# Kernel optimization log

Measured on AMD Instinct MI355X. Metric: run time of the kernel, lower is better.

## Reference

```python
import jax, jax.numpy as jnp
import numpy as np

TAU = 0.6      # similarity threshold in tokenwise_interpolation
TOPK = 3       # top-k candidates
ALPHA = 0.5    # interpolation weight (module default self.alpha)
EPS = 1e-12    # F.normalize eps


def _l2norm(x):
    n = jnp.linalg.norm(x, axis=-1, keepdims=True)
    return x / jnp.maximum(n, EPS)


def _mh_rms(x, gamma):
    # SparseMultiHeadRMSNorm: F.normalize over last dim, * gamma * sqrt(dim)
    dim = x.shape[-1]
    return _l2norm(x) * gamma * (dim ** 0.5)


def _match_and_copy(sim, k_flat, v_flat, k_side, v_side):
    topv, topi = jax.lax.top_k(sim, min(TOPK, sim.shape[1]))
    valid = topv[:, 0] > TAU                      # [N]
    kg = k_side[topi[:, 0]]                       # gather best match
    vg = v_side[topi[:, 0]]
    k_out = jnp.where(valid[:, None], kg, k_flat)
    v_out = jnp.where(valid[:, None], vg, v_flat)
    return k_out, v_out


def setup_inputs() -> dict:
    key = jax.random.key(0)
    ks = jax.random.split(key, 8)
    N, H, C = 4096, 16, 64
    D = H * C
    inp = {
        'x':  jax.random.normal(ks[0], (N, D), jnp.float32),
        'k0': jax.random.normal(ks[1], (N, H, C), jnp.float32),
        'v0': jax.random.normal(ks[2], (N, H, C), jnp.float32),
        'k1': jax.random.normal(ks[3], (N, H, C), jnp.float32),
        'v1': jax.random.normal(ks[4], (N, H, C), jnp.float32),
        'W_qkv': jax.random.normal(ks[5], (D, 3 * D), jnp.float32) * 0.02,
        'b_qkv': jnp.zeros((3 * D,), jnp.float32),
        'gamma_q': jnp.ones((H, C), jnp.float32),
        'gamma_k': jnp.ones((H, C), jnp.float32),
        'W_out': jax.random.normal(ks[6], (D, D), jnp.float32) * 0.02,
        'b_out': jnp.zeros((D,), jnp.float32),
    }
    return inp


def reference(x, k0, v0, k1, v1, W_qkv, b_qkv, gamma_q, gamma_k, W_out, b_out):
    N, D = x.shape
    H, C = gamma_q.shape

    # fused QKV projection -> (N, 3, H, C)
    qkv = (x @ W_qkv + b_qkv).reshape(N, 3, H, C)
    q, k, v = qkv[:, 0], qkv[:, 1], qkv[:, 2]

    # q RMS norm
    q = _mh_rms(q, gamma_q)

    # tokenwise interpolation: cosine top-k matching against stores
    k_flat, v_flat = k.reshape(N, D), v.reshape(N, D)
    k0f, v0f = k0.reshape(-1, D), v0.reshape(-1, D)
    k1f, v1f = k1.reshape(-1, D), v1.reshape(-1, D)
    kbn = _l2norm(k_flat)
    sim0 = kbn @ _l2norm(k0f).T        # [N, N0]
    sim1 = kbn @ _l2norm(k1f).T        # [N, N1]
    k_out0, v_out0 = _match_and_copy(sim0, k_flat, v_flat, k0f, v0f)
    k_out1, v_out1 = _match_and_copy(sim1, k_flat, v_flat, k1f, v1f)

    # combine with residual and detached norm rescale
    combined_k = (1.0 - ALPHA) * k_out0 + ALPHA * k_out1 + k_flat
    sk = jax.lax.stop_gradient(jnp.linalg.norm(k_flat) / jnp.linalg.norm(combined_k))
    k_out = (combined_k * sk).reshape(N, H, C)
    combined_v = (1.0 - ALPHA) * v_out0 + ALPHA * v_out1 + v_flat
    sv = jax.lax.stop_gradient(jnp.linalg.norm(v_flat) / jnp.linalg.norm(combined_v))
    v_out = (combined_v * sv).reshape(N, H, C)

    # k RMS norm after interpolation
    k_out = _mh_rms(k_out, gamma_k)

    # full scaled dot-product attention (single sparse batch => one sequence)
    scores = jnp.einsum('nhc,mhc->hnm', q, k_out) / (C ** 0.5)
    attn = jax.nn.softmax(scores, axis=-1)
    h = jnp.einsum('hnm,mhc->nhc', attn, v_out).reshape(N, D)

    return h @ W_out + b_out
```

## Files before the change

kernel.cpp:

```cpp
#include <hip/hip_runtime.h>
#include <math.h>

#define TAU_F 0.6f

typedef short short8 __attribute__((ext_vector_type(8)));
typedef float floatx4 __attribute__((ext_vector_type(4)));
typedef int   intx4  __attribute__((ext_vector_type(4)));

__device__ __forceinline__ ushort f2bf(float f) {
    unsigned u = __float_as_uint(f);
    u += 0x7FFF + ((u >> 16) & 1);
    return (ushort)(u >> 16);
}
__device__ __forceinline__ float bf2f(ushort h) {
    return __uint_as_float(((unsigned)h) << 16);
}
__device__ __forceinline__ int swz(int row, int j, int mask) { return j ^ (row & mask); }

__device__ __forceinline__ unsigned cvt_pk_bf16(float lo, float hi) {
    unsigned r;
    asm("v_cvt_pk_bf16_f32 %0, %1, %2" : "=v"(r) : "v"(lo), "v"(hi));
    return r;
}
__device__ __forceinline__ float exp2_fast(float x) {
    float r; asm("v_exp_f32 %0, %1" : "=v"(r) : "v"(x)); return r;
}

template<int CPR, int SC, int NW = 4>
__device__ __forceinline__ void stage_swz(void* lds, const char* g, int rowstride_bytes,
                                          int w, int lane)
{
    #pragma unroll
    for (int p = 0; p < (SC + NW - 1) / NW; ++p) {
        int sc = w + p * NW;
        if (SC % NW != 0 && sc >= SC) break;
        int LC = sc * 64 + lane;
        int r = LC / CPR;
        int s = LC % CPR;
        int j = s ^ (r & (CPR - 1));
        const char* gp = g + (size_t)r * rowstride_bytes + j * 16;
        __builtin_amdgcn_global_load_lds(
            (const __attribute__((address_space(1))) void*)gp,
            (__attribute__((address_space(3))) void*)((char*)lds + sc * 1024), 16, 0, 0);
    }
}

__global__ __launch_bounds__(256) void gemm_nt_kernel(
    const ushort* __restrict__ Ah, int lda,
    const ushort* __restrict__ Bh, int ldb,
    const float* __restrict__ bias, float* __restrict__ C, int ldc, int K)
{
    __shared__ __align__(16) ushort As_h[128 * 32];
    __shared__ __align__(16) ushort Bs_h[128 * 32];
    const int tid = threadIdx.x;
    const int w = tid >> 6, lane = tid & 63;
    const int quad = lane >> 4, c15 = lane & 15;
    const int wm = w >> 1, wn = w & 1;
    const int bm = blockIdx.y * 128, bn = blockIdx.x * 128;

    floatx4 acc[4][4];
    #pragma unroll
    for (int i = 0; i < 4; i++)
        #pragma unroll
        for (int j = 0; j < 4; j++) acc[i][j] = (floatx4){0.f, 0.f, 0.f, 0.f};

    const char* Ab = (const char*)(Ah + (size_t)bm * lda);
    const char* Bb = (const char*)(Bh + (size_t)bn * ldb);

    for (int k0 = 0; k0 < K; k0 += 32) {
        stage_swz<4, 8>(As_h, Ab + k0 * 2, lda * 2, w, lane);
        stage_swz<4, 8>(Bs_h, Bb + k0 * 2, ldb * 2, w, lane);
        __syncthreads();
        short8 a_h[4], b_h[4];
        #pragma unroll
        for (int mt = 0; mt < 4; mt++) {
            int row = wm * 64 + mt * 16 + c15;
            a_h[mt] = *(const short8*)&As_h[row * 32 + swz(row, quad, 3) * 8];
        }
        #pragma unroll
        for (int nt = 0; nt < 4; nt++) {
            int row = wn * 64 + nt * 16 + c15;
            b_h[nt] = *(const short8*)&Bs_h[row * 32 + swz(row, quad, 3) * 8];
        }
        #pragma unroll
        for (int mt = 0; mt < 4; mt++)
            #pragma unroll
            for (int nt = 0; nt < 4; nt++)
                acc[mt][nt] = __builtin_amdgcn_mfma_f32_16x16x32_bf16(a_h[mt], b_h[nt], acc[mt][nt], 0, 0, 0);
        __syncthreads();
    }
    #pragma unroll
    for (int mt = 0; mt < 4; mt++)
        #pragma unroll
        for (int nt = 0; nt < 4; nt++) {
            int col = bn + wn * 64 + nt * 16 + c15;
            float bs = bias ? bias[col] : 0.f;
            #pragma unroll
            for (int r = 0; r < 4; r++) {
                int row = bm + wm * 64 + mt * 16 + quad * 4 + r;
                C[(size_t)row * ldc + col] = acc[mt][nt][r] + bs;
            }
        }
}

__global__ __launch_bounds__(256) void gemm_nt64_kernel(
    const ushort* __restrict__ Ah, int lda,
    const ushort* __restrict__ Bh, int ldb,
    const float* __restrict__ bias, float* __restrict__ C, int ldc, int K)
{
    __shared__ __align__(16) ushort As_h[128 * 32];
    __shared__ __align__(16) ushort Bs_h[64 * 32];
    const int tid = threadIdx.x;
    const int w = tid >> 6, lane = tid & 63;
    const int quad = lane >> 4, c15 = lane & 15;
    const int wm = w >> 1, wn = w & 1;
    const int bm = blockIdx.y * 128, bn = blockIdx.x * 64;

    floatx4 acc[4][2];
    #pragma unroll
    for (int i = 0; i < 4; i++)
        #pragma unroll
        for (int j = 0; j < 2; j++) acc[i][j] = (floatx4){0.f, 0.f, 0.f, 0.f};

    const char* Ab = (const char*)(Ah + (size_t)bm * lda);
    const char* Bb = (const char*)(Bh + (size_t)bn * ldb);

    for (int k0 = 0; k0 < K; k0 += 32) {
        stage_swz<4, 8>(As_h, Ab + k0 * 2, lda * 2, w, lane);
        stage_swz<4, 4>(Bs_h, Bb + k0 * 2, ldb * 2, w, lane);
        __syncthreads();
        short8 a_h[4], b_h[2];
        #pragma unroll
        for (int mt = 0; mt < 4; mt++) {
            int row = wm * 64 + mt * 16 + c15;
            a_h[mt] = *(const short8*)&As_h[row * 32 + swz(row, quad, 3) * 8];
        }
        #pragma unroll
        for (int nt = 0; nt < 2; nt++) {
            int row = wn * 32 + nt * 16 + c15;
            b_h[nt] = *(const short8*)&Bs_h[row * 32 + swz(row, quad, 3) * 8];
        }
        #pragma unroll
        for (int mt = 0; mt < 4; mt++)
            #pragma unroll
            for (int nt = 0; nt < 2; nt++)
                acc[mt][nt] = __builtin_amdgcn_mfma_f32_16x16x32_bf16(a_h[mt], b_h[nt], acc[mt][nt], 0, 0, 0);
        __syncthreads();
    }
    #pragma unroll
    for (int mt = 0; mt < 4; mt++)
        #pragma unroll
        for (int nt = 0; nt < 2; nt++) {
            int col = bn + wn * 32 + nt * 16 + c15;
            float bs = bias ? bias[col] : 0.f;
            #pragma unroll
            for (int r = 0; r < 4; r++) {
                int row = bm + wm * 64 + mt * 16 + quad * 4 + r;
                C[(size_t)row * ldc + col] = acc[mt][nt][r] + bs;
            }
        }
}

__global__ __launch_bounds__(256) void simmax_i8(
    const char* __restrict__ A, const char* __restrict__ B,
    float* __restrict__ pval, int* __restrict__ pidx)
{
    __shared__ __align__(16) char As_b[128 * 64];
    __shared__ __align__(16) char Bs_b[128 * 64];
    __shared__ float redv[128][2];
    __shared__ int   redi[128][2];
    const int tid = threadIdx.x;
    const int w = tid >> 6, lane = tid & 63;
    const int quad = lane >> 4, c15 = lane & 15;
    const int wm = w >> 1, wn = w & 1;
    const int bm = blockIdx.y * 128, bn = blockIdx.x * 128;

    intx4 acc[4][4];
    #pragma unroll
    for (int i = 0; i < 4; i++)
        #pragma unroll
        for (int j = 0; j < 4; j++) acc[i][j] = (intx4){0, 0, 0, 0};

    const char* Ab = A + (size_t)bm * 1024;
    const char* Bb = B + (size_t)bn * 1024;

    for (int k0 = 0; k0 < 1024; k0 += 64) {
        stage_swz<4, 8>(As_b, Ab + k0, 1024, w, lane);
        stage_swz<4, 8>(Bs_b, Bb + k0, 1024, w, lane);
        __syncthreads();
        intx4 a_f[4], b_f[4];
        #pragma unroll
        for (int mt = 0; mt < 4; mt++) {
            int row = wm * 64 + mt * 16 + c15;
            a_f[mt] = *(const intx4*)&As_b[row * 64 + swz(row, quad, 3) * 16];
        }
        #pragma unroll
        for (int nt = 0; nt < 4; nt++) {
            int row = wn * 64 + nt * 16 + c15;
            b_f[nt] = *(const intx4*)&Bs_b[row * 64 + swz(row, quad, 3) * 16];
        }
        #pragma unroll
        for (int mt = 0; mt < 4; mt++)
            #pragma unroll
            for (int nt = 0; nt < 4; nt++)
                acc[mt][nt] = __builtin_amdgcn_mfma_i32_16x16x64_i8(a_f[mt], b_f[nt], acc[mt][nt], 0, 0, 0);
        __syncthreads();
    }
    const float isc = 1.0f / 16129.0f;
    #pragma unroll
    for (int mt = 0; mt < 4; mt++)
        #pragma unroll
        for (int r = 0; r < 4; r++) {
            float bv = -1e30f; int bi = 0;
            #pragma unroll
            for (int nt = 0; nt < 4; nt++) {
                float v = (float)acc[mt][nt][r] * isc;
                int col = bn + wn * 64 + nt * 16 + c15;
                if (v > bv) { bv = v; bi = col; }
            }
            #pragma unroll
            for (int m = 1; m < 16; m <<= 1) {
                float ov = __shfl_xor(bv, m, 64);
                int   oi = __shfl_xor(bi, m, 64);
                if (ov > bv || (ov == bv && oi < bi)) { bv = ov; bi = oi; }
            }
            if (c15 == 0) {
                int row = wm * 64 + mt * 16 + quad * 4 + r;
                redv[row][wn] = bv; redi[row][wn] = bi;
            }
        }
    __syncthreads();
    if (tid < 128) {
        float v0 = redv[tid][0], v1 = redv[tid][1];
        int   i0 = redi[tid][0], i1 = redi[tid][1];
        bool t = (v1 > v0) || (v1 == v0 && i1 < i0);
        pval[(size_t)blockIdx.x * 4096 + bm + tid] = t ? v1 : v0;
        pidx[(size_t)blockIdx.x * 4096 + bm + tid] = t ? i1 : i0;
    }
}

__global__ void simreduce2_kernel(const float* __restrict__ pval, const int* __restrict__ pidx,
                                  float* __restrict__ bv0, int* __restrict__ bi0,
                                  float* __restrict__ bv1, int* __restrict__ bi1)
{
    const int n = blockIdx.x * 256 + threadIdx.x;
    float best = -1e30f; int besti = 0x7fffffff;
    for (int c = 0; c < 32; c++) {
        float v = pval[(size_t)c * 4096 + n]; int ix = pidx[(size_t)c * 4096 + n];
        if (v > best || (v == best && ix < besti)) { best = v; besti = ix; }
    }
    bv0[n] = best; bi0[n] = besti;
    best = -1e30f; besti = 0x7fffffff;
    for (int c = 32; c < 64; c++) {
        float v = pval[(size_t)c * 4096 + n]; int ix = pidx[(size_t)c * 4096 + n];
        if (v > best || (v == best && ix < besti)) { best = v; besti = ix; }
    }
    bv1[n] = best; bi1[n] = besti - 4096;
}

__global__ __launch_bounds__(256) void xconv_kernel(const float* __restrict__ s,
                                                    ushort* __restrict__ dh)
{
    const int i = blockIdx.x * 256 + threadIdx.x;
    float4 v = ((const float4*)s)[i];
    ushort4 h;
    h.x = f2bf(v.x); h.y = f2bf(v.y); h.z = f2bf(v.z); h.w = f2bf(v.w);
    ((ushort4*)dh)[i] = h;
}

__global__ __launch_bounds__(256) void wtrans_kernel(const float* __restrict__ src, int R, int Cc,
                                                     ushort* __restrict__ dh)
{
    __shared__ float t[64][65];
    const int tid = threadIdx.x;
    const int c0 = blockIdx.x * 64, r0 = blockIdx.y * 64;
    #pragma unroll
    for (int i = 0; i < 16; i++) {
        int lin = i * 256 + tid;
        int rr = lin >> 6, cc = lin & 63;
        t[rr][cc] = src[(size_t)(r0 + rr) * Cc + c0 + cc];
    }
    __syncthreads();
    #pragma unroll
    for (int i = 0; i < 16; i++) {
        int lin = i * 256 + tid;
        int cc2 = lin >> 6, rr2 = lin & 63;
        dh[(size_t)(c0 + cc2) * R + r0 + rr2] = f2bf(t[rr2][cc2]);
    }
}

__device__ __forceinline__ char q127(float v) {
    float c = fminf(fmaxf(v * 127.0f, -127.0f), 127.0f);
    return (char)__float2int_rn(c);
}

__global__ __launch_bounds__(256) void prep_kernel(const float* __restrict__ QKV,
                                                   const float* __restrict__ k0,
                                                   const float* __restrict__ k1,
                                                   const float* __restrict__ gamma_q,
                                                   char* __restrict__ kq,
                                                   char* __restrict__ k01q,
                                                   ushort* __restrict__ Qbh)
{
    const int n = blockIdx.x, t = threadIdx.x, y = blockIdx.y;
    if (y == 3) {
        float4 v = ((const float4*)(QKV + (size_t)n * 3072))[t];
        float hs = v.x * v.x + v.y * v.y + v.z * v.z + v.w * v.w;
        #pragma unroll
        for (int m = 1; m < 16; m <<= 1) hs += __shfl_xor(hs, m, 64);
        float inv = 8.0f / fmaxf(sqrtf(hs), 1e-12f);
        float4 g = ((const float4*)gamma_q)[t];
        const int h = t >> 4;
        size_t o = ((size_t)h * 4096 + n) * 64 + 4 * (t & 15);
        ushort4 hh;
        hh.x = f2bf(v.x * inv * g.x);
        hh.y = f2bf(v.y * inv * g.y);
        hh.z = f2bf(v.z * inv * g.z);
        hh.w = f2bf(v.w * inv * g.w);
        *(ushort4*)(Qbh + o) = hh;
        return;
    }
    const float* src; int ld; char* dst;
    if (y == 0)      { src = QKV + 1024; ld = 3072; dst = kq; }
    else if (y == 1) { src = k0; ld = 1024; dst = k01q; }
    else             { src = k1; ld = 1024; dst = k01q + (size_t)4096 * 1024; }
    float4 v = *(const float4*)(src + (size_t)n * ld + 4 * t);
    float ss = v.x * v.x + v.y * v.y + v.z * v.z + v.w * v.w;
    #pragma unroll
    for (int off = 32; off; off >>= 1) ss += __shfl_xor(ss, off, 64);
    __shared__ float wsum[4];
    if ((t & 63) == 0) wsum[t >> 6] = ss;
    __syncthreads();
    float inv = 1.0f / fmaxf(sqrtf(wsum[0] + wsum[1] + wsum[2] + wsum[3]), 1e-12f);
    char4 o;
    o.x = q127(v.x * inv); o.y = q127(v.y * inv);
    o.z = q127(v.z * inv); o.w = q127(v.w * inv);
    *(char4*)(dst + (size_t)n * 1024 + 4 * t) = o;
}

__global__ __launch_bounds__(256) void combine_kernel(
    const float* __restrict__ QKV,
    const float* __restrict__ k0, const float* __restrict__ v0,
    const float* __restrict__ k1, const float* __restrict__ v1,
    const float* __restrict__ bv0, const int* __restrict__ bi0,
    const float* __restrict__ bv1, const int* __restrict__ bi1,
    const float* __restrict__ gamma_k,
    ushort* __restrict__ CKh,
    float* __restrict__ CV, float* __restrict__ pps)
{
    const int n = blockIdx.x, t = threadIdx.x;
    const bool va0 = bv0[n] > TAU_F; const int i0 = bi0[n];
    const bool va1 = bv1[n] > TAU_F; const int i1 = bi1[n];
    float4 kf = ((const float4*)(QKV + (size_t)n * 3072 + 1024))[t];
    float4 vf = ((const float4*)(QKV + (size_t)n * 3072 + 2048))[t];
    float4 kg0 = va0 ? ((const float4*)(k0 + (size_t)i0 * 1024))[t] : kf;
    float4 vg0 = va0 ? ((const float4*)(v0 + (size_t)i0 * 1024))[t] : vf;
    float4 kg1 = va1 ? ((const float4*)(k1 + (size_t)i1 * 1024))[t] : kf;
    float4 vg1 = va1 ? ((const float4*)(v1 + (size_t)i1 * 1024))[t] : vf;
    float4 ck, cv;
    ck.x = 0.5f * kg0.x + 0.5f * kg1.x + kf.x;
    ck.y = 0.5f * kg0.y + 0.5f * kg1.y + kf.y;
    ck.z = 0.5f * kg0.z + 0.5f * kg1.z + kf.z;
    ck.w = 0.5f * kg0.w + 0.5f * kg1.w + kf.w;
    cv.x = 0.5f * vg0.x + 0.5f * vg1.x + vf.x;
    cv.y = 0.5f * vg0.y + 0.5f * vg1.y + vf.y;
    cv.z = 0.5f * vg0.z + 0.5f * vg1.z + vf.z;
    cv.w = 0.5f * vg0.w + 0.5f * vg1.w + vf.w;
    ((float4*)(CV + (size_t)n * 1024))[t] = cv;
    float s0 = vf.x * vf.x + vf.y * vf.y + vf.z * vf.z + vf.w * vf.w;
    float s1 = cv.x * cv.x + cv.y * cv.y + cv.z * cv.z + cv.w * cv.w;
    #pragma unroll
    for (int off = 32; off; off >>= 1) {
        s0 += __shfl_xor(s0, off, 64);
        s1 += __shfl_xor(s1, off, 64);
    }
    __shared__ float w0[4], w1[4];
    if ((t & 63) == 0) { w0[t >> 6] = s0; w1[t >> 6] = s1; }
    float hs = ck.x * ck.x + ck.y * ck.y + ck.z * ck.z + ck.w * ck.w;
    #pragma unroll
    for (int m = 1; m < 16; m <<= 1) hs += __shfl_xor(hs, m, 64);
    float inv = 8.0f / fmaxf(sqrtf(hs), 1e-12f);
    float4 g = ((const float4*)gamma_k)[t];
    const int h = t >> 4;
    size_t o = ((size_t)h * 4096 + n) * 64 + 4 * (t & 15);
    ushort4 hh;
    hh.x = f2bf(ck.x * inv * g.x);
    hh.y = f2bf(ck.y * inv * g.y);
    hh.z = f2bf(ck.z * inv * g.z);
    hh.w = f2bf(ck.w * inv * g.w);
    *(ushort4*)(CKh + o) = hh;
    __syncthreads();
    if (t == 0) {
        pps[n]        = w0[0] + w0[1] + w0[2] + w0[3];
        pps[4096 + n] = w1[0] + w1[1] + w1[2] + w1[3];
    }
}

__global__ __launch_bounds__(256) void sumred_kernel(const float* __restrict__ pps,
                                                     float* __restrict__ ss)
{
    const int t = threadIdx.x;
    float a = 0.f, b = 0.f;
    #pragma unroll 4
    for (int i = t; i < 4096; i += 256) { a += pps[i]; b += pps[4096 + i]; }
    #pragma unroll
    for (int off = 32; off; off >>= 1) {
        a += __shfl_xor(a, off, 64);
        b += __shfl_xor(b, off, 64);
    }
    __shared__ float sa[4], sb[4];
    if ((t & 63) == 0) { sa[t >> 6] = a; sb[t >> 6] = b; }
    __syncthreads();
    if (t == 0) {
        ss[0] = sa[0] + sa[1] + sa[2] + sa[3];
        ss[1] = sb[0] + sb[1] + sb[2] + sb[3];
    }
}

__global__ __launch_bounds__(256) void vt_kernel(const float* __restrict__ CV,
                                                 const float* __restrict__ ss,
                                                 ushort* __restrict__ Vt)
{
    __shared__ float t[64][65];
    const float sv = sqrtf(ss[0] / ss[1]);
    const int tid = threadIdx.x;
    const int n0 = blockIdx.x * 64, d0 = blockIdx.y * 64;
    #pragma unroll
    for (int i = 0; i < 16; i++) {
        int lin = i * 256 + tid;
        int r = lin >> 6, c = lin & 63;
        t[r][c] = CV[(size_t)(n0 + r) * 1024 + d0 + c];
    }
    __syncthreads();
    #pragma unroll
    for (int i = 0; i < 16; i++) {
        int lin = i * 256 + tid;
        int dr = lin >> 6, nc = lin & 63;
        Vt[(size_t)(d0 + dr) * 4096 + n0 + nc] = f2bf(t[nc][dr] * sv);
    }
}

__global__ __launch_bounds__(512, 6) void attn_mfma(
    const ushort* __restrict__ Qh,
    const ushort* __restrict__ Kh,
    const ushort* __restrict__ Vt,
    ushort* __restrict__ Hb)
{
    __shared__ __align__(16) ushort Ks[2][64 * 64];
    __shared__ __align__(16) ushort Vs[2][64 * 64];
    __shared__ __align__(16) ushort Ps[128 * 64];
    const int h = blockIdx.y;
    const int n0 = blockIdx.x * 128;
    const int tid = threadIdx.x;
    const int w = tid >> 6, lane = tid & 63;
    const int quad = lane >> 4, c15 = lane & 15;

    short8 qf[2];
    #pragma unroll
    for (int kh = 0; kh < 2; kh++)
        qf[kh] = *(const short8*)(Qh + ((size_t)h * 4096 + n0 + w * 16 + c15) * 64 + kh * 32 + quad * 8);

    floatx4 po[4];
    #pragma unroll
    for (int nt = 0; nt < 4; nt++) po[nt] = (floatx4){0.f, 0.f, 0.f, 0.f};
    float lsum = 0.f;

    const float KSC = 0.18033688011112042f;
    const float KBI = -12.262907847556189f;

    const int prow = w * 16 + c15;
    const ushort* Kbase = Kh + (size_t)h * 4096 * 64;
    const ushort* Vbase = Vt + (size_t)h * 64 * 4096;

    stage_swz<8, 8, 8>(Ks[0], (const char*)(Kbase + 0), 128, w, lane);
    stage_swz<8, 8, 8>(Vs[0], (const char*)(Vbase + 0), 8192, w, lane);
    __syncthreads();

    int cur = 0;
    for (int it = 0; it < 64; ++it) {
        if (it + 1 < 64) {
            const int m1 = (it + 1) * 64;
            stage_swz<8, 8, 8>(Ks[cur ^ 1], (const char*)(Kbase + (size_t)m1 * 64), 128, w, lane);
            stage_swz<8, 8, 8>(Vs[cur ^ 1], (const char*)(Vbase + m1), 8192, w, lane);
        }
        const ushort* Kc = Ks[cur];
        const ushort* Vc = Vs[cur];

        floatx4 s[4];
        #pragma unroll
        for (int nt = 0; nt < 4; nt++) {
            int rk = nt * 16 + c15;
            short8 ka = *(const short8*)&Kc[rk * 64 + swz(rk, quad, 7) * 8];
            short8 kb = *(const short8*)&Kc[rk * 64 + swz(rk, 4 + quad, 7) * 8];
            floatx4 z = (floatx4){0.f, 0.f, 0.f, 0.f};
            z = __builtin_amdgcn_mfma_f32_16x16x32_bf16(ka, qf[0], z, 0, 0, 0);
            z = __builtin_amdgcn_mfma_f32_16x16x32_bf16(kb, qf[1], z, 0, 0, 0);
            s[nt] = z;
        }
        #pragma unroll
        for (int nt = 0; nt < 4; nt++) {
            float p0 = exp2_fast(fmaf(s[nt][0], KSC, KBI));
            float p1 = exp2_fast(fmaf(s[nt][1], KSC, KBI));
            float p2 = exp2_fast(fmaf(s[nt][2], KSC, KBI));
            float p3 = exp2_fast(fmaf(s[nt][3], KSC, KBI));
            lsum += (p0 + p1) + (p2 + p3);
            uint2 pk;
            pk.x = cvt_pk_bf16(p0, p1);
            pk.y = cvt_pk_bf16(p2, p3);
            int ch = (nt * 4 + quad) ^ ((prow & 7) << 1);
            *(uint2*)&Ps[prow * 64 + ch * 4] = pk;
        }
        __builtin_amdgcn_wave_barrier();
        #pragma unroll
        for (int kb2 = 0; kb2 < 2; kb2++) {
            short8 pa = *(const short8*)&Ps[prow * 64 + swz(prow, kb2 * 4 + quad, 7) * 8];
            #pragma unroll
            for (int nt = 0; nt < 4; nt++) {
                int dr = nt * 16 + c15;
                int j = kb2 * 4 + quad;
                short8 vb = *(const short8*)&Vc[dr * 64 + swz(dr, j, 7) * 8];
                po[nt] = __builtin_amdgcn_mfma_f32_16x16x32_bf16(pa, vb, po[nt], 0, 0, 0);
            }
        }
        __syncthreads();
        cur ^= 1;
    }
    float l = lsum;
    l += __shfl_xor(l, 16, 64);
    l += __shfl_xor(l, 32, 64);
    #pragma unroll
    for (int r = 0; r < 4; r++) {
        float lr = __shfl(l, quad * 4 + r, 64);
        float inv = 1.0f / lr;
        int row = n0 + w * 16 + quad * 4 + r;
        #pragma unroll
        for (int nt = 0; nt < 4; nt++)
            Hb[(size_t)row * 1024 + h * 64 + nt * 16 + c15] = f2bf(po[nt][r] * inv);
    }
}

extern "C" void kernel_launch(void* const* d_in, const int* in_sizes, int n_in,
                              void* d_out, int out_size, void* d_ws, size_t ws_size,
                              hipStream_t stream)
{
    const float* x       = (const float*)d_in[0];
    const float* k0      = (const float*)d_in[1];
    const float* v0      = (const float*)d_in[2];
    const float* k1      = (const float*)d_in[3];
    const float* v1      = (const float*)d_in[4];
    const float* W_qkv   = (const float*)d_in[5];
    const float* b_qkv   = (const float*)d_in[6];
    const float* gamma_q = (const float*)d_in[7];
    const float* gamma_k = (const float*)d_in[8];
    const float* W_out   = (const float*)d_in[9];
    const float* b_out   = (const float*)d_in[10];
    float* out = (float*)d_out;

    char* W = (char*)d_ws;
    float*  QKV = (float*)(W + 0);
    ushort* Vt  = (ushort*)(W + 0);
    ushort* Hb  = (ushort*)(W + 8388608);
    ushort* Qbh = (ushort*)(W + 50331648);
    ushort* xh   = (ushort*)(W + 67108864);
    ushort* Wqh  = (ushort*)(W + 67108864 + 8388608);
    char*   kq   = (char*)(W + 67108864);
    char*   k01q = (char*)(W + 67108864 + 4194304);
    float*  pval = (float*)(W + 67108864 + 25165824);
    int*    pidx = (int*)  (W + 67108864 + 26214400);
    float*  CV   = (float*)(W + 67108864);
    ushort* CKh  = (ushort*)(W + 67108864 + 16777216);
    ushort* Wob  = (ushort*)(W + 67108864);
    float* bv0  = (float*)(W + 100663296);
    int*   bi0  = (int*)  (W + 100663296 + 16384);
    float* bv1  = (float*)(W + 100663296 + 32768);
    int*   bi1  = (int*)  (W + 100663296 + 49152);
    float* ssum = (float*)(W + 100663296 + 65536);
    float* pps  = (float*)(W + 100663296 + 131072);

    xconv_kernel<<<4096, 256, 0, stream>>>(x, xh);
    wtrans_kernel<<<dim3(48, 16), 256, 0, stream>>>(W_qkv, 1024, 3072, Wqh);
    gemm_nt_kernel<<<dim3(24, 32), 256, 0, stream>>>(xh, 1024, Wqh, 1024,
                                                     b_qkv, QKV, 3072, 1024);
    prep_kernel<<<dim3(4096, 4), 256, 0, stream>>>(QKV, k0, k1, gamma_q, kq, k01q, Qbh);
    simmax_i8<<<dim3(64, 32), 256, 0, stream>>>(kq, k01q, pval, pidx);
    simreduce2_kernel<<<16, 256, 0, stream>>>(pval, pidx, bv0, bi0, bv1, bi1);
    combine_kernel<<<4096, 256, 0, stream>>>(QKV, k0, v0, k1, v1, bv0, bi0, bv1, bi1,
                                             gamma_k, CKh, CV, pps);
    sumred_kernel<<<1, 256, 0, stream>>>(pps, ssum);
    vt_kernel<<<dim3(64, 16), 256, 0, stream>>>(CV, ssum, Vt);
    wtrans_kernel<<<dim3(16, 16), 256, 0, stream>>>(W_out, 1024, 1024, Wob);
    attn_mfma<<<dim3(32, 16), 512, 0, stream>>>(Qbh, CKh, Vt, Hb);
    gemm_nt64_kernel<<<dim3(16, 32), 256, 0, stream>>>(Hb, 1024, Wob, 1024,
                                                       b_out, out, 1024, 1024);
}
```

Before: 404.3 us.

## Process two 16-row query groups per wave in attention, halving block threads

The attention kernel now runs 4 waves of 256 threads per block instead of 8 waves, and each wave handles 32 query rows as two 16-row groups. Each K and V fragment read from LDS therefore feeds two MFMAs. This roughly halves LDS read traffic per FLOP and the staging work per thread stays the same in total. In exchange it needs more registers per wave (double accumulators and scores), has fewer waves to hide latency, and the launch bounds change to (256,2), which may lower occupancy.

```diff
diff --git a/kernel.cpp b/kernel.cpp
--- a/kernel.cpp
+++ b/kernel.cpp
@@ -440,7 +440,7 @@
     }
 }
 
-__global__ __launch_bounds__(512, 6) void attn_mfma(
+__global__ __launch_bounds__(256, 2) void attn_mfma(
     const ushort* __restrict__ Qh,
     const ushort* __restrict__ Kh,
     const ushort* __restrict__ Vt,
@@ -455,87 +455,105 @@
     const int w = tid >> 6, lane = tid & 63;
     const int quad = lane >> 4, c15 = lane & 15;
 
-    short8 qf[2];
-    #pragma unroll
-    for (int kh = 0; kh < 2; kh++)
-        qf[kh] = *(const short8*)(Qh + ((size_t)h * 4096 + n0 + w * 16 + c15) * 64 + kh * 32 + quad * 8);
-
-    floatx4 po[4];
-    #pragma unroll
-    for (int nt = 0; nt < 4; nt++) po[nt] = (floatx4){0.f, 0.f, 0.f, 0.f};
-    float lsum = 0.f;
+    short8 qf[2][2];
+    #pragma unroll
+    for (int g = 0; g < 2; g++)
+        #pragma unroll
+        for (int kh = 0; kh < 2; kh++)
+            qf[g][kh] = *(const short8*)(Qh + ((size_t)h * 4096 + n0 + w * 32 + g * 16 + c15) * 64
+                                         + kh * 32 + quad * 8);
+
+    floatx4 po[2][4];
+    #pragma unroll
+    for (int g = 0; g < 2; g++)
+        #pragma unroll
+        for (int nt = 0; nt < 4; nt++) po[g][nt] = (floatx4){0.f, 0.f, 0.f, 0.f};
+    float lsum[2] = {0.f, 0.f};
 
     const float KSC = 0.18033688011112042f;
     const float KBI = -12.262907847556189f;
 
-    const int prow = w * 16 + c15;
+    const int pr0 = w * 32 + c15;
     const ushort* Kbase = Kh + (size_t)h * 4096 * 64;
     const ushort* Vbase = Vt + (size_t)h * 64 * 4096;
 
-    stage_swz<8, 8, 8>(Ks[0], (const char*)(Kbase + 0), 128, w, lane);
-    stage_swz<8, 8, 8>(Vs[0], (const char*)(Vbase + 0), 8192, w, lane);
+    stage_swz<8, 8, 4>(Ks[0], (const char*)(Kbase + 0), 128, w, lane);
+    stage_swz<8, 8, 4>(Vs[0], (const char*)(Vbase + 0), 8192, w, lane);
     __syncthreads();
 
     int cur = 0;
     for (int it = 0; it < 64; ++it) {
         if (it + 1 < 64) {
             const int m1 = (it + 1) * 64;
-            stage_swz<8, 8, 8>(Ks[cur ^ 1], (const char*)(Kbase + (size_t)m1 * 64), 128, w, lane);
-            stage_swz<8, 8, 8>(Vs[cur ^ 1], (const char*)(Vbase + m1), 8192, w, lane);
+            stage_swz<8, 8, 4>(Ks[cur ^ 1], (const char*)(Kbase + (size_t)m1 * 64), 128, w, lane);
+            stage_swz<8, 8, 4>(Vs[cur ^ 1], (const char*)(Vbase + m1), 8192, w, lane);
         }
         const ushort* Kc = Ks[cur];
         const ushort* Vc = Vs[cur];
 
-        floatx4 s[4];
+        floatx4 s[2][4];
         #pragma unroll
         for (int nt = 0; nt < 4; nt++) {
             int rk = nt * 16 + c15;
             short8 ka = *(const short8*)&Kc[rk * 64 + swz(rk, quad, 7) * 8];
             short8 kb = *(const short8*)&Kc[rk * 64 + swz(rk, 4 + quad, 7) * 8];
-            floatx4 z = (floatx4){0.f, 0.f, 0.f, 0.f};
-            z = __builtin_amdgcn_mfma_f32_16x16x32_bf16(ka, qf[0], z, 0, 0, 0);
-            z = __builtin_amdgcn_mfma_f32_16x16x32_bf16(kb, qf[1], z, 0, 0, 0);
-            s[nt] = z;
-        }
-        #pragma unroll
-        for (int nt = 0; nt < 4; nt++) {
-            float p0 = exp2_fast(fmaf(s[nt][0], KSC, KBI));
-            float p1 = exp2_fast(fmaf(s[nt][1], KSC, KBI));
-            float p2 = exp2_fast(fmaf(s[nt][2], KSC, KBI));
-            float p3 = exp2_fast(fmaf(s[nt][3], KSC, KBI));
-            lsum += (p0 + p1) + (p2 + p3);
-            uint2 pk;
-            pk.x = cvt_pk_bf16(p0, p1);
-            pk.y = cvt_pk_bf16(p2, p3);
-            int ch = (nt * 4 + quad) ^ ((prow & 7) << 1);
-            *(uint2*)&Ps[prow * 64 + ch * 4] = pk;
+            floatx4 z0 = (floatx4){0.f, 0.f, 0.f, 0.f};
+            floatx4 z1 = (floatx4){0.f, 0.f, 0.f, 0.f};
+            z0 = __builtin_amdgcn_mfma_f32_16x16x32_bf16(ka, qf[0][0], z0, 0, 0, 0);
+            z0 = __builtin_amdgcn_mfma_f32_16x16x32_bf16(kb, qf[0][1], z0, 0, 0, 0);
+            z1 = __builtin_amdgcn_mfma_f32_16x16x32_bf16(ka, qf[1][0], z1, 0, 0, 0);
+            z1 = __builtin_amdgcn_mfma_f32_16x16x32_bf16(kb, qf[1][1], z1, 0, 0, 0);
+            s[0][nt] = z0;
+            s[1][nt] = z1;
+        }
+        #pragma unroll
+        for (int g = 0; g < 2; g++) {
+            const int prg = pr0 + g * 16;
+            #pragma unroll
+            for (int nt = 0; nt < 4; nt++) {
+                float p0 = exp2_fast(fmaf(s[g][nt][0], KSC, KBI));
+                float p1 = exp2_fast(fmaf(s[g][nt][1], KSC, KBI));
+                float p2 = exp2_fast(fmaf(s[g][nt][2], KSC, KBI));
+                float p3 = exp2_fast(fmaf(s[g][nt][3], KSC, KBI));
+                lsum[g] += (p0 + p1) + (p2 + p3);
+                uint2 pk;
+                pk.x = cvt_pk_bf16(p0, p1);
+                pk.y = cvt_pk_bf16(p2, p3);
+                int ch = (nt * 4 + quad) ^ ((prg & 7) << 1);
+                *(uint2*)&Ps[prg * 64 + ch * 4] = pk;
+            }
         }
         __builtin_amdgcn_wave_barrier();
         #pragma unroll
         for (int kb2 = 0; kb2 < 2; kb2++) {
-            short8 pa = *(const short8*)&Ps[prow * 64 + swz(prow, kb2 * 4 + quad, 7) * 8];
+            short8 pa0 = *(const short8*)&Ps[pr0 * 64 + swz(pr0, kb2 * 4 + quad, 7) * 8];
+            short8 pa1 = *(const short8*)&Ps[(pr0 + 16) * 64 + swz(pr0 + 16, kb2 * 4 + quad, 7) * 8];
             #pragma unroll
             for (int nt = 0; nt < 4; nt++) {
                 int dr = nt * 16 + c15;
                 int j = kb2 * 4 + quad;
                 short8 vb = *(const short8*)&Vc[dr * 64 + swz(dr, j, 7) * 8];
-                po[nt] = __builtin_amdgcn_mfma_f32_16x16x32_bf16(pa, vb, po[nt], 0, 0, 0);
+                po[0][nt] = __builtin_amdgcn_mfma_f32_16x16x32_bf16(pa0, vb, po[0][nt], 0, 0, 0);
+                po[1][nt] = __builtin_amdgcn_mfma_f32_16x16x32_bf16(pa1, vb, po[1][nt], 0, 0, 0);
             }
         }
         __syncthreads();
         cur ^= 1;
     }
-    float l = lsum;
-    l += __shfl_xor(l, 16, 64);
-    l += __shfl_xor(l, 32, 64);
-    #pragma unroll
-    for (int r = 0; r < 4; r++) {
-        float lr = __shfl(l, quad * 4 + r, 64);
-        float inv = 1.0f / lr;
-        int row = n0 + w * 16 + quad * 4 + r;
-        #pragma unroll
-        for (int nt = 0; nt < 4; nt++)
-            Hb[(size_t)row * 1024 + h * 64 + nt * 16 + c15] = f2bf(po[nt][r] * inv);
+    #pragma unroll
+    for (int g = 0; g < 2; g++) {
+        float l = lsum[g];
+        l += __shfl_xor(l, 16, 64);
+        l += __shfl_xor(l, 32, 64);
+        #pragma unroll
+        for (int r = 0; r < 4; r++) {
+            float lr = __shfl(l, quad * 4 + r, 64);
+            float inv = 1.0f / lr;
+            int row = n0 + w * 32 + g * 16 + quad * 4 + r;
+            #pragma unroll
+            for (int nt = 0; nt < 4; nt++)
+                Hb[(size_t)row * 1024 + h * 64 + nt * 16 + c15] = f2bf(po[g][nt][r] * inv);
+        }
     }
 }
 
@@ -589,7 +607,7 @@
     sumred_kernel<<<1, 256, 0, stream>>>(pps, ssum);
     vt_kernel<<<dim3(64, 16), 256, 0, stream>>>(CV, ssum, Vt);
     wtrans_kernel<<<dim3(16, 16), 256, 0, stream>>>(W_out, 1024, 1024, Wob);
-    attn_mfma<<<dim3(32, 16), 512, 0, stream>>>(Qbh, CKh, Vt, Hb);
+    attn_mfma<<<dim3(32, 16), 256, 0, stream>>>(Qbh, CKh, Vt, Hb);
     gemm_nt64_kernel<<<dim3(16, 32), 256, 0, stream>>>(Hb, 1024, Wob, 1024,
                                                        b_out, out, 1024, 1024);
 }
```

Result: slower. 421.1 us (+4.2%).

## Unroll attention K/V double buffer with static LDS buffers and remap blocks

Applied to the files above, without the earlier changes.

The attention kernel's ping-pong loop is unrolled by two, so each half uses a fixed, compile-time LDS buffer, with K and V staging written as direct global_load_lds calls whose addresses are precomputed once. Block indices are remapped so consecutive workgroups spread across heads in an interleaved order, which may improve L2 locality or distribution across XCDs. The aim is to cut address arithmetic and dynamic buffer selection in the inner loop. The remapping assumes a fixed grid of 32x16 blocks.

```diff
diff --git a/kernel.cpp b/kernel.cpp
--- a/kernel.cpp
+++ b/kernel.cpp
@@ -446,11 +446,13 @@
     const ushort* __restrict__ Vt,
     ushort* __restrict__ Hb)
 {
-    __shared__ __align__(16) ushort Ks[2][64 * 64];
-    __shared__ __align__(16) ushort Vs[2][64 * 64];
+    __shared__ __align__(16) ushort Ks0[64 * 64], Ks1[64 * 64];
+    __shared__ __align__(16) ushort Vs0[64 * 64], Vs1[64 * 64];
     __shared__ __align__(16) ushort Ps[128 * 64];
-    const int h = blockIdx.y;
-    const int n0 = blockIdx.x * 128;
+    const int idl = blockIdx.y * 32 + blockIdx.x;
+    const int nid = (idl & 7) * 64 + (idl >> 3);
+    const int h = nid >> 5;
+    const int n0 = (nid & 31) * 128;
     const int tid = threadIdx.x;
     const int w = tid >> 6, lane = tid & 63;
     const int quad = lane >> 4, c15 = lane & 15;
@@ -469,62 +471,77 @@
     const float KBI = -12.262907847556189f;
 
     const int prow = w * 16 + c15;
-    const ushort* Kbase = Kh + (size_t)h * 4096 * 64;
-    const ushort* Vbase = Vt + (size_t)h * 64 * 4096;
-
-    stage_swz<8, 8, 8>(Ks[0], (const char*)(Kbase + 0), 128, w, lane);
-    stage_swz<8, 8, 8>(Vs[0], (const char*)(Vbase + 0), 8192, w, lane);
+
+    const int LC = w * 64 + lane;
+    const int sr = LC >> 3, sj = (LC & 7) ^ (sr & 7);
+    const char* kg = (const char*)(Kh + (size_t)h * 4096 * 64) + (size_t)sr * 128 + sj * 16;
+    const char* vg = (const char*)(Vt + (size_t)h * 64 * 4096) + (size_t)sr * 8192 + sj * 16;
+
+#define STAGE2(KDST, VDST, T)                                                        \
+    do {                                                                             \
+        __builtin_amdgcn_global_load_lds(                                            \
+            (const __attribute__((address_space(1))) void*)(kg + (size_t)(T) * 8192),\
+            (__attribute__((address_space(3))) void*)((char*)(KDST) + w * 1024),     \
+            16, 0, 0);                                                               \
+        __builtin_amdgcn_global_load_lds(                                            \
+            (const __attribute__((address_space(1))) void*)(vg + (size_t)(T) * 128), \
+            (__attribute__((address_space(3))) void*)((char*)(VDST) + w * 1024),     \
+            16, 0, 0);                                                               \
+    } while (0)
+
+#define BODY(KC, VC)                                                                 \
+    do {                                                                             \
+        floatx4 s_[4];                                                               \
+        _Pragma("unroll")                                                            \
+        for (int nt = 0; nt < 4; nt++) {                                             \
+            int rk = nt * 16 + c15;                                                  \
+            short8 ka = *(const short8*)&KC[rk * 64 + swz(rk, quad, 7) * 8];         \
+            short8 kb = *(const short8*)&KC[rk * 64 + swz(rk, 4 + quad, 7) * 8];     \
+            floatx4 z = (floatx4){0.f, 0.f, 0.f, 0.f};                               \
+            z = __builtin_amdgcn_mfma_f32_16x16x32_bf16(ka, qf[0], z, 0, 0, 0);      \
+            z = __builtin_amdgcn_mfma_f32_16x16x32_bf16(kb, qf[1], z, 0, 0, 0);      \
+            s_[nt] = z;                                                              \
+        }                                                                            \
+        _Pragma("unroll")                                                            \
+        for (int nt = 0; nt < 4; nt++) {                                             \
+            float p0 = exp2_fast(fmaf(s_[nt][0], KSC, KBI));                         \
+            float p1 = exp2_fast(fmaf(s_[nt][1], KSC, KBI));                         \
+            float p2 = exp2_fast(fmaf(s_[nt][2], KSC, KBI));                         \
+            float p3 = exp2_fast(fmaf(s_[nt][3], KSC, KBI));                         \
+            lsum += (p0 + p1) + (p2 + p3);                                           \
+            uint2 pk;                                                                \
+            pk.x = cvt_pk_bf16(p0, p1);                                              \
+            pk.y = cvt_pk_bf16(p2, p3);                                              \
+            int ch = (nt * 4 + quad) ^ ((prow & 7) << 1);                            \
+            *(uint2*)&Ps[prow * 64 + ch * 4] = pk;                                   \
+        }                                                                            \
+        __builtin_amdgcn_wave_barrier();                                             \
+        _Pragma("unroll")                                                            \
+        for (int kb2 = 0; kb2 < 2; kb2++) {                                          \
+            short8 pa = *(const short8*)&Ps[prow * 64 + swz(prow, kb2 * 4 + quad, 7) * 8]; \
+            _Pragma("unroll")                                                        \
+            for (int nt = 0; nt < 4; nt++) {                                         \
+                int dr = nt * 16 + c15;                                              \
+                short8 vb = *(const short8*)&VC[dr * 64 + swz(dr, kb2 * 4 + quad, 7) * 8]; \
+                po[nt] = __builtin_amdgcn_mfma_f32_16x16x32_bf16(pa, vb, po[nt], 0, 0, 0); \
+            }                                                                        \
+        }                                                                            \
+    } while (0)
+
+    STAGE2(Ks0, Vs0, 0);
     __syncthreads();
 
-    int cur = 0;
-    for (int it = 0; it < 64; ++it) {
-        if (it + 1 < 64) {
-            const int m1 = (it + 1) * 64;
-            stage_swz<8, 8, 8>(Ks[cur ^ 1], (const char*)(Kbase + (size_t)m1 * 64), 128, w, lane);
-            stage_swz<8, 8, 8>(Vs[cur ^ 1], (const char*)(Vbase + m1), 8192, w, lane);
-        }
-        const ushort* Kc = Ks[cur];
-        const ushort* Vc = Vs[cur];
-
-        floatx4 s[4];
-        #pragma unroll
-        for (int nt = 0; nt < 4; nt++) {
-            int rk = nt * 16 + c15;
-            short8 ka = *(const short8*)&Kc[rk * 64 + swz(rk, quad, 7) * 8];
-            short8 kb = *(const short8*)&Kc[rk * 64 + swz(rk, 4 + quad, 7) * 8];
-            floatx4 z = (floatx4){0.f, 0.f, 0.f, 0.f};
-            z = __builtin_amdgcn_mfma_f32_16x16x32_bf16(ka, qf[0], z, 0, 0, 0);
-            z = __builtin_amdgcn_mfma_f32_16x16x32_bf16(kb, qf[1], z, 0, 0, 0);
-            s[nt] = z;
-        }
-        #pragma unroll
-        for (int nt = 0; nt < 4; nt++) {
-            float p0 = exp2_fast(fmaf(s[nt][0], KSC, KBI));
-            float p1 = exp2_fast(fmaf(s[nt][1], KSC, KBI));
-            float p2 = exp2_fast(fmaf(s[nt][2], KSC, KBI));
-            float p3 = exp2_fast(fmaf(s[nt][3], KSC, KBI));
-            lsum += (p0 + p1) + (p2 + p3);
-            uint2 pk;
-            pk.x = cvt_pk_bf16(p0, p1);
-            pk.y = cvt_pk_bf16(p2, p3);
-            int ch = (nt * 4 + quad) ^ ((prow & 7) << 1);
-            *(uint2*)&Ps[prow * 64 + ch * 4] = pk;
-        }
-        __builtin_amdgcn_wave_barrier();
-        #pragma unroll
-        for (int kb2 = 0; kb2 < 2; kb2++) {
-            short8 pa = *(const short8*)&Ps[prow * 64 + swz(prow, kb2 * 4 + quad, 7) * 8];
-            #pragma unroll
-            for (int nt = 0; nt < 4; nt++) {
-                int dr = nt * 16 + c15;
-                int j = kb2 * 4 + quad;
-                short8 vb = *(const short8*)&Vc[dr * 64 + swz(dr, j, 7) * 8];
-                po[nt] = __builtin_amdgcn_mfma_f32_16x16x32_bf16(pa, vb, po[nt], 0, 0, 0);
-            }
-        }
-        __syncthreads();
-        cur ^= 1;
-    }
+    for (int it = 0; it < 64; it += 2) {
+        STAGE2(Ks1, Vs1, it + 1);
+        BODY(Ks0, Vs0);
+        __syncthreads();
+        if (it + 2 < 64) STAGE2(Ks0, Vs0, it + 2);
+        BODY(Ks1, Vs1);
+        __syncthreads();
+    }
+#undef STAGE2
+#undef BODY
+
     float l = lsum;
     l += __shfl_xor(l, 16, 64);
     l += __shfl_xor(l, 32, 64);
```

After: 402.4 us. No clear change (-0.5%).
